# Kernel tuning notes

Hardware: AMD Instinct MI355X
Metric: run time of the kernel (lower is better)

The kernel has to match this reference:

```python
import jax, jax.numpy as jnp
import numpy as np

B, T, C = 4, 2048, 1024
H = 16
D = C // H  # head_dim = 64

def setup_inputs() -> dict:
    key = jax.random.key(0)
    k1, k2, k3 = jax.random.split(key, 3)
    s = 1.0 / np.sqrt(C)
    x = jax.random.normal(k1, (B, T, C), dtype=jnp.float32)
    w_qkv = jax.random.normal(k2, (C, 3 * C), dtype=jnp.float32) * s
    w_proj = jax.random.normal(k3, (C, C), dtype=jnp.float32) * s
    b_proj = jnp.zeros((C,), dtype=jnp.float32)
    return {"x": x, "w_qkv": w_qkv, "w_proj": w_proj, "b_proj": b_proj}

def reference(x, w_qkv, w_proj, b_proj):
    Bc, Tc, Cc = x.shape
    scale = 1.0 / np.sqrt(D)
    qkv = x @ w_qkv                       # [B,T,3C]
    q, k, v = jnp.split(qkv, 3, axis=-1)  # each [B,T,C]
    def heads(t):
        return t.reshape(Bc, Tc, H, D).transpose(0, 2, 1, 3)  # [B,H,T,D]
    q, k, v = heads(q), heads(k), heads(v)
    attn = jnp.einsum('bhqd,bhkd->bhqk', q, k) * scale        # [B,H,T,T]
    causal = jnp.tril(jnp.ones((Tc, Tc), dtype=bool))
    attn = jnp.where(causal, attn, -jnp.inf)
    attn = jax.nn.softmax(attn, axis=-1)
    out = jnp.einsum('bhqk,bhkd->bhqd', attn, v)              # [B,H,T,D]
    out = out.transpose(0, 2, 1, 3).reshape(Bc, Tc, Cc)
    return out @ w_proj + b_proj
```

## Files before the change

kernel.cpp:

```cpp
#include <hip/hip_runtime.h>

typedef unsigned short u16;
typedef unsigned int u32;
typedef __attribute__((ext_vector_type(8))) __bf16 bf16x8;
typedef __attribute__((ext_vector_type(4))) float f32x4;
typedef __attribute__((ext_vector_type(16))) float f32x16;
typedef __attribute__((ext_vector_type(8))) unsigned short ushort8;
typedef __attribute__((ext_vector_type(4))) unsigned short ushort4v;
typedef __attribute__((ext_vector_type(4))) unsigned int u32x4;
typedef __attribute__((ext_vector_type(4))) float float4v;

#define B_ 4
#define T_ 2048
#define C_ 1024
#define H_ 16
#define D_ 64
#define M_ (B_ * T_)

union ABUn { ushort8 u; bf16x8 b; };

__device__ __forceinline__ u16 f2bf(float f) {
  u32 u = __builtin_bit_cast(u32, f);
  u32 r = u + 0x7fffu + ((u >> 16) & 1u);
  return (u16)(r >> 16);
}

__device__ __forceinline__ float fexp2(float x) {
  float r; asm("v_exp_f32 %0, %1" : "=v"(r) : "v"(x)); return r;
}

__device__ __forceinline__ u32 pkbf(float lo, float hi_) {
  u32 r; asm("v_cvt_pk_bf16_f32 %0, %1, %2" : "=v"(r) : "v"(lo), "v"(hi_)); return r;
}

__device__ __forceinline__ void gl16(const u16* g, u16* l) {
  __builtin_amdgcn_global_load_lds((const __attribute__((address_space(1))) void*)g,
                                   (__attribute__((address_space(3))) void*)l, 16, 0, 0);
}

__global__ void cast_kernel(const float* __restrict__ in, u16* __restrict__ out, int n4) {
  int i = blockIdx.x * blockDim.x + threadIdx.x;
  if (i >= n4) return;
  float4v v = ((const float4v*)in)[i];
  ushort4v o;
  o[0] = f2bf(v[0]); o[1] = f2bf(v[1]); o[2] = f2bf(v[2]); o[3] = f2bf(v[3]);
  ((ushort4v*)out)[i] = o;
}

__global__ void transpose_cast_kernel(const float* __restrict__ src, u16* __restrict__ dst,
                                      int Kd, int Nd) {
  __shared__ float tile[32][33];
  int n0 = blockIdx.x * 32, k0 = blockIdx.y * 32;
  int tx = threadIdx.x, ty = threadIdx.y;
#pragma unroll
  for (int i = 0; i < 32; i += 8)
    tile[ty + i][tx] = src[(k0 + ty + i) * Nd + n0 + tx];
  __syncthreads();
#pragma unroll
  for (int i = 0; i < 32; i += 8)
    dst[(n0 + ty + i) * Kd + k0 + tx] = f2bf(tile[tx][ty + i]);
}

template <int EPI>
__global__ __launch_bounds__(256, 2) void gemm_bt(
    const u16* __restrict__ A, const u16* __restrict__ Bt,
    u16* __restrict__ Qb, u16* __restrict__ Kb, u16* __restrict__ Vb,
    float* __restrict__ Out, const float* __restrict__ bias) {
  __shared__ u16 As[128 * 64];
  __shared__ u16 Bs[128 * 64];
  const int tid = threadIdx.x;
  const int lane = tid & 63, wave = tid >> 6;
  const int wm = wave >> 1, wn = wave & 1;
  const int lg = lane >> 4, lr = lane & 15;
  const int m0 = blockIdx.y * 128, n0 = blockIdx.x * 128;

  f32x4 acc[4][4];
  const f32x4 zero = {0.0f, 0.0f, 0.0f, 0.0f};
#pragma unroll
  for (int mi = 0; mi < 4; ++mi)
#pragma unroll
    for (int ni = 0; ni < 4; ++ni) acc[mi][ni] = zero;

  const u16* Abase = A + m0 * 1024;
  const u16* Bbase = Bt + n0 * 1024;
  int aoff[4];
#pragma unroll
  for (int j = 0; j < 4; ++j) {
    int s = wave * 256 + j * 64 + lane;
    int row = s >> 3, sp = s & 7;
    aoff[j] = row * 1024 + (sp ^ (row & 7)) * 8;
  }
  char* AsB = (char*)As;
  char* BsB = (char*)Bs;

  for (int k0 = 0; k0 < 1024; k0 += 64) {
#pragma unroll
    for (int j = 0; j < 4; ++j) {
      u16* ldst_a = &As[(wave * 256 + j * 64) * 8];
      u16* ldst_b = &Bs[(wave * 256 + j * 64) * 8];
      gl16(Abase + aoff[j] + k0, ldst_a);
      gl16(Bbase + aoff[j] + k0, ldst_b);
    }
    __syncthreads();
#pragma unroll
    for (int kk = 0; kk < 2; ++kk) {
      bf16x8 am[4], bn[4];
#pragma unroll
      for (int mi = 0; mi < 4; ++mi) {
        int row = wm * 64 + mi * 16 + lr;
        ABUn u;
        u.u = *(const ushort8*)(AsB + ((u32)(row * 128 + ((kk * 64 + lg * 16) ^ ((row & 7) << 4)))));
        am[mi] = u.b;
      }
#pragma unroll
      for (int ni = 0; ni < 4; ++ni) {
        int row = wn * 64 + ni * 16 + lr;
        ABUn u;
        u.u = *(const ushort8*)(BsB + ((u32)(row * 128 + ((kk * 64 + lg * 16) ^ ((row & 7) << 4)))));
        bn[ni] = u.b;
      }
#pragma unroll
      for (int mi = 0; mi < 4; ++mi)
#pragma unroll
        for (int ni = 0; ni < 4; ++ni)
          acc[mi][ni] = __builtin_amdgcn_mfma_f32_16x16x32_bf16(am[mi], bn[ni], acc[mi][ni], 0, 0, 0);
    }
    __syncthreads();
  }

#pragma unroll
  for (int mi = 0; mi < 4; ++mi)
#pragma unroll
    for (int ni = 0; ni < 4; ++ni) {
      int m = m0 + wm * 64 + mi * 16 + lg * 4;
      int n = n0 + wn * 64 + ni * 16 + lr;
      if (EPI == 0) {
        int part = n >> 10, c = n & 1023;
        int h = c >> 6, d = c & 63;
        int b = m >> 11, t = m & 2047;
        if (part == 2) {
          ushort4v pv;
#pragma unroll
          for (int r = 0; r < 4; ++r) pv[r] = f2bf(acc[mi][ni][r]);
          *(ushort4v*)&Vb[((b * H_ + h) * D_ + d) * T_ + t] = pv;
        } else {
#pragma unroll
          for (int r = 0; r < 4; ++r) {
            float v = acc[mi][ni][r];
            if (part == 0)
              Qb[((b * H_ + h) * T_ + t + r) * D_ + d] = f2bf(v * 0.18033688f);
            else
              Kb[((b * H_ + h) * T_ + t + r) * D_ + d] = f2bf(v);
          }
        }
      } else {
#pragma unroll
        for (int r = 0; r < 4; ++r)
          Out[(m + r) * 1024 + n] = acc[mi][ni][r] + bias[n];
      }
    }
}

__global__ __launch_bounds__(256, 4) void attn_kernel(
    const u16* __restrict__ Qb, const u16* __restrict__ Kb,
    const u16* __restrict__ Vt, u16* __restrict__ Ob) {
  __shared__ u16 smem[4][4096];
  const int bh = blockIdx.y;
  const int tid = threadIdx.x;
  const int lane = tid & 63, wave = tid >> 6;
  const int hi = lane >> 5, ln = lane & 31;
  const int hh = bh & (H_ - 1), bb = bh >> 4;

  const u16* Qh = Qb + bh * (T_ * D_);
  const u16* Kh = Kb + bh * (T_ * D_);
  const u16* Vh = Vt + bh * (T_ * D_);
  const int slot0 = wave * 128;

  int srow[2], scol[2];
#pragma unroll
  for (int j = 0; j < 2; ++j) {
    int slot = slot0 + j * 64 + lane;
    srow[j] = slot >> 3;
    scol[j] = (slot & 7) ^ (srow[j] & 7);
  }

#pragma unroll
  for (int pass = 0; pass < 2; ++pass) {
    const int q0 = pass ? (1920 - (int)blockIdx.x * 128) : ((int)blockIdx.x * 128);
    const int qw0 = q0 + wave * 32;

    bf16x8 qf[4];
    {
      const u16* qr = Qh + (qw0 + ln) * 64 + hi * 8;
#pragma unroll
      for (int ks = 0; ks < 4; ++ks)
        qf[ks] = __builtin_bit_cast(bf16x8, *(const ushort8*)(qr + ks * 16));
    }

    f32x16 o[2];
#pragma unroll
    for (int dt = 0; dt < 2; ++dt)
#pragma unroll
      for (int i = 0; i < 16; ++i) o[dt][i] = 0.0f;
    float m = -1e30f, l = 0.0f;

    const int nchunk = q0 / 64 + 2;

    __syncthreads();
#pragma unroll
    for (int j = 0; j < 2; ++j) {
      gl16(Kh + srow[j] * 64 + scol[j] * 8, &smem[0][(slot0 + j * 64) * 8]);
      gl16(Vh + srow[j] * 2048 + scol[j] * 8, &smem[2][(slot0 + j * 64) * 8]);
    }
    __syncthreads();

    for (int ch = 0; ch < nchunk; ++ch) {
      const int kv0 = ch * 64;
      const int cur = ch & 1;
      if (ch + 1 < nchunk) {
        const int kn = kv0 + 64;
#pragma unroll
        for (int j = 0; j < 2; ++j) {
          gl16(Kh + (kn + srow[j]) * 64 + scol[j] * 8, &smem[cur ^ 1][(slot0 + j * 64) * 8]);
          gl16(Vh + srow[j] * 2048 + kn + scol[j] * 8, &smem[2 + (cur ^ 1)][(slot0 + j * 64) * 8]);
        }
      }
      if (kv0 <= qw0 + 31) {
        const char* Kc = (const char*)smem[cur];
        const char* Vc = (const char*)smem[2 + cur];
        f32x16 s0, s1;
#pragma unroll
        for (int i = 0; i < 16; ++i) { s0[i] = 0.0f; s1[i] = 0.0f; }
        __builtin_amdgcn_s_setprio(1);
#pragma unroll
        for (int ks = 0; ks < 4; ++ks) {
          int r0 = ln, r1 = 32 + ln;
          bf16x8 kf0 = __builtin_bit_cast(bf16x8,
              *(const ushort8*)(Kc + r0 * 128 + (u32)((ks * 32 + hi * 16) ^ ((r0 & 7) << 4))));
          bf16x8 kf1 = __builtin_bit_cast(bf16x8,
              *(const ushort8*)(Kc + r1 * 128 + (u32)((ks * 32 + hi * 16) ^ ((r1 & 7) << 4))));
          s0 = __builtin_amdgcn_mfma_f32_32x32x16_bf16(kf0, qf[ks], s0, 0, 0, 0);
          s1 = __builtin_amdgcn_mfma_f32_32x32x16_bf16(kf1, qf[ks], s1, 0, 0, 0);
        }
        __builtin_amdgcn_s_setprio(0);

        const int qg = qw0 + ln;
        if ((kv0 + 63) > qw0) {
#pragma unroll
          for (int r = 0; r < 16; ++r) {
            int R = (r & 3) + 8 * (r >> 2) + 4 * hi;
            s0[r] = (kv0 + R > qg) ? -1e30f : s0[r];
            s1[r] = (kv0 + 32 + R > qg) ? -1e30f : s1[r];
          }
        }
        float mx[8];
#pragma unroll
        for (int i = 0; i < 8; ++i)
          mx[i] = fmaxf(fmaxf(s0[i], s0[i + 8]), fmaxf(s1[i], s1[i + 8]));
#pragma unroll
        for (int i = 0; i < 4; ++i) mx[i] = fmaxf(mx[i], mx[i + 4]);
        float cm = fmaxf(fmaxf(mx[0], mx[1]), fmaxf(mx[2], mx[3]));
        cm = fmaxf(cm, __shfl_xor(cm, 32));
        float mn = fmaxf(m, cm);
        float fsc = fexp2(m - mn);
        m = mn;
#pragma unroll
        for (int r = 0; r < 16; ++r) {
          s0[r] = fexp2(s0[r] - mn);
          s1[r] = fexp2(s1[r] - mn);
        }
        float sm[8];
#pragma unroll
        for (int i = 0; i < 8; ++i) sm[i] = (s0[i] + s0[i + 8]) + (s1[i] + s1[i + 8]);
#pragma unroll
        for (int i = 0; i < 4; ++i) sm[i] += sm[i + 4];
        float ssum = (sm[0] + sm[1]) + (sm[2] + sm[3]);
        ssum += __shfl_xor(ssum, 32);
        l = l * fsc + ssum;
#pragma unroll
        for (int dt = 0; dt < 2; ++dt)
#pragma unroll
          for (int i = 0; i < 16; ++i) o[dt][i] *= fsc;

        bf16x8 pb[4];
#pragma unroll
        for (int sub = 0; sub < 2; ++sub) {
          u32 a0, a1, a2, a3, a4, a5, a6, a7;
          if (sub == 0) {
            a0 = pkbf(s0[0], s0[1]);  a1 = pkbf(s0[2], s0[3]);
            a2 = pkbf(s0[4], s0[5]);  a3 = pkbf(s0[6], s0[7]);
            a4 = pkbf(s0[8], s0[9]);  a5 = pkbf(s0[10], s0[11]);
            a6 = pkbf(s0[12], s0[13]); a7 = pkbf(s0[14], s0[15]);
          } else {
            a0 = pkbf(s1[0], s1[1]);  a1 = pkbf(s1[2], s1[3]);
            a2 = pkbf(s1[4], s1[5]);  a3 = pkbf(s1[6], s1[7]);
            a4 = pkbf(s1[8], s1[9]);  a5 = pkbf(s1[10], s1[11]);
            a6 = pkbf(s1[12], s1[13]); a7 = pkbf(s1[14], s1[15]);
          }
          asm volatile("v_permlane32_swap_b32 %0, %1" : "+v"(a0), "+v"(a2));
          asm volatile("v_permlane32_swap_b32 %0, %1" : "+v"(a1), "+v"(a3));
          asm volatile("v_permlane32_swap_b32 %0, %1" : "+v"(a4), "+v"(a6));
          asm volatile("v_permlane32_swap_b32 %0, %1" : "+v"(a5), "+v"(a7));
          u32x4 w0, w1;
          w0[0] = a0; w0[1] = a1; w0[2] = a2; w0[3] = a3;
          w1[0] = a4; w1[1] = a5; w1[2] = a6; w1[3] = a7;
          pb[sub * 2 + 0] = __builtin_bit_cast(bf16x8, w0);
          pb[sub * 2 + 1] = __builtin_bit_cast(bf16x8, w1);
        }
        __builtin_amdgcn_s_setprio(1);
#pragma unroll
        for (int dt = 0; dt < 2; ++dt) {
          int r = dt * 32 + ln;
          u32 rs = (u32)((r & 7) << 4);
#pragma unroll
          for (int ks = 0; ks < 4; ++ks) {
            bf16x8 vfk = __builtin_bit_cast(bf16x8,
                *(const ushort8*)(Vc + r * 128 + (u32)((ks * 32 + hi * 16) ^ rs)));
            o[dt] = __builtin_amdgcn_mfma_f32_32x32x16_bf16(vfk, pb[ks], o[dt], 0, 0, 0);
          }
        }
        __builtin_amdgcn_s_setprio(0);
      }
      __syncthreads();
    }

    __syncthreads();
    char* Wb = (char*)smem[wave];
    {
      float inv = 1.0f / l;
      int q = ln;
      u32 rs = (u32)((q & 7) << 4);
#pragma unroll
      for (int dt = 0; dt < 2; ++dt)
#pragma unroll
        for (int p = 0; p < 8; ++p) {
          u32 w = pkbf(o[dt][2 * p] * inv, o[dt][2 * p + 1] * inv);
          int d = dt * 32 + ((2 * p) & 3) + 8 * (p >> 1) + 4 * hi;
          *(u32*)(Wb + ((u32)(q * 128 + d * 2) ^ rs)) = w;
        }
    }
    asm volatile("s_waitcnt lgkmcnt(0)" ::: "memory");
#pragma unroll
    for (int j = 0; j < 4; ++j) {
      int idx = j * 64 + lane;
      int row = idx >> 3, sp = idx & 7;
      ushort8 v = *(const ushort8*)(Wb + row * 128 + (u32)((sp * 16) ^ ((row & 7) << 4)));
      *(ushort8*)(Ob + (bb * T_ + qw0 + row) * C_ + hh * 64 + sp * 8) = v;
    }
  }
}

extern "C" void kernel_launch(void* const* d_in, const int* in_sizes, int n_in,
                              void* d_out, int out_size, void* d_ws, size_t ws_size,
                              hipStream_t stream) {
  const float* x = (const float*)d_in[0];
  const float* w_qkv = (const float*)d_in[1];
  const float* w_proj = (const float*)d_in[2];
  const float* b_proj = (const float*)d_in[3];
  float* out = (float*)d_out;

  char* ws = (char*)d_ws;
  u16* xb = (u16*)(ws);
  u16* wqT = (u16*)(ws + 16777216);
  u16* wpT = (u16*)(ws + 16777216 + 6291456);
  u16* Qb = (u16*)(ws + 25165824);
  u16* Kb = (u16*)(ws + 25165824 + 16777216);
  u16* Vt = (u16*)(ws + 25165824 + 2 * 16777216);
  u16* Ob = xb;

  cast_kernel<<<(M_ * C_ / 4 + 255) / 256, 256, 0, stream>>>(x, xb, M_ * C_ / 4);
  dim3 tb(32, 8);
  transpose_cast_kernel<<<dim3(3 * C_ / 32, C_ / 32), tb, 0, stream>>>(w_qkv, wqT, C_, 3 * C_);
  transpose_cast_kernel<<<dim3(C_ / 32, C_ / 32), tb, 0, stream>>>(w_proj, wpT, C_, C_);

  gemm_bt<0><<<dim3(3 * C_ / 128, M_ / 128), 256, 0, stream>>>(
      xb, wqT, Qb, Kb, Vt, nullptr, nullptr);

  attn_kernel<<<dim3(T_ / 256, B_ * H_), 256, 0, stream>>>(Qb, Kb, Vt, Ob);

  gemm_bt<1><<<dim3(C_ / 128, M_ / 128), 256, 0, stream>>>(
      Ob, wpT, nullptr, nullptr, nullptr, out, b_proj);
}
```

Before: 250.0 us.

## Double attention block to 8 waves and add lazy softmax rescaling

Each attention workgroup now runs 512 threads (8 waves) covering 256 query rows per pass, so each K/V chunk staged into shared memory is shared by twice as many waves, with one load per thread per chunk instead of two. The online softmax skips the max update and the rescale of the output accumulators and row sum unless some lane's chunk max exceeds the running max by more than 8 (in log2 units), which cuts exp and multiply work. The trade-offs are fewer workgroups and more idle waves from causal imbalance inside larger blocks. The lazy rescale also lets unnormalised values grow by up to 2^8 before correction, which is safe in fp32 but changes the numerics slightly.

```diff
diff --git a/kernel.cpp b/kernel.cpp
--- a/kernel.cpp
+++ b/kernel.cpp
@@ -161,7 +161,7 @@
     }
 }
 
-__global__ __launch_bounds__(256, 4) void attn_kernel(
+__global__ __launch_bounds__(512, 4) void attn_kernel(
     const u16* __restrict__ Qb, const u16* __restrict__ Kb,
     const u16* __restrict__ Vt, u16* __restrict__ Ob) {
   __shared__ u16 smem[4][4096];
@@ -174,19 +174,14 @@
   const u16* Qh = Qb + bh * (T_ * D_);
   const u16* Kh = Kb + bh * (T_ * D_);
   const u16* Vh = Vt + bh * (T_ * D_);
-  const int slot0 = wave * 128;
-
-  int srow[2], scol[2];
-#pragma unroll
-  for (int j = 0; j < 2; ++j) {
-    int slot = slot0 + j * 64 + lane;
-    srow[j] = slot >> 3;
-    scol[j] = (slot & 7) ^ (srow[j] & 7);
-  }
+
+  const int srow = tid >> 3;
+  const int scol = (tid & 7) ^ (srow & 7);
+  u16* kdst = &smem[0][(wave * 64) * 8];
 
 #pragma unroll
   for (int pass = 0; pass < 2; ++pass) {
-    const int q0 = pass ? (1920 - (int)blockIdx.x * 128) : ((int)blockIdx.x * 128);
+    const int q0 = pass ? (1792 - (int)blockIdx.x * 256) : ((int)blockIdx.x * 256);
     const int qw0 = q0 + wave * 32;
 
     bf16x8 qf[4];
@@ -204,14 +199,11 @@
       for (int i = 0; i < 16; ++i) o[dt][i] = 0.0f;
     float m = -1e30f, l = 0.0f;
 
-    const int nchunk = q0 / 64 + 2;
-
-    __syncthreads();
-#pragma unroll
-    for (int j = 0; j < 2; ++j) {
-      gl16(Kh + srow[j] * 64 + scol[j] * 8, &smem[0][(slot0 + j * 64) * 8]);
-      gl16(Vh + srow[j] * 2048 + scol[j] * 8, &smem[2][(slot0 + j * 64) * 8]);
-    }
+    const int nchunk = q0 / 64 + 4;
+
+    __syncthreads();
+    gl16(Kh + srow * 64 + scol * 8, kdst);
+    gl16(Vh + srow * 2048 + scol * 8, kdst + 2 * 4096);
     __syncthreads();
 
     for (int ch = 0; ch < nchunk; ++ch) {
@@ -219,11 +211,8 @@
       const int cur = ch & 1;
       if (ch + 1 < nchunk) {
         const int kn = kv0 + 64;
-#pragma unroll
-        for (int j = 0; j < 2; ++j) {
-          gl16(Kh + (kn + srow[j]) * 64 + scol[j] * 8, &smem[cur ^ 1][(slot0 + j * 64) * 8]);
-          gl16(Vh + srow[j] * 2048 + kn + scol[j] * 8, &smem[2 + (cur ^ 1)][(slot0 + j * 64) * 8]);
-        }
+        gl16(Kh + (kn + srow) * 64 + scol * 8, kdst + (cur ^ 1) * 4096);
+        gl16(Vh + srow * 2048 + kn + scol * 8, kdst + (2 + (cur ^ 1)) * 4096);
       }
       if (kv0 <= qw0 + 31) {
         const char* Kc = (const char*)smem[cur];
@@ -261,13 +250,20 @@
         for (int i = 0; i < 4; ++i) mx[i] = fmaxf(mx[i], mx[i + 4]);
         float cm = fmaxf(fmaxf(mx[0], mx[1]), fmaxf(mx[2], mx[3]));
         cm = fmaxf(cm, __shfl_xor(cm, 32));
-        float mn = fmaxf(m, cm);
-        float fsc = fexp2(m - mn);
-        m = mn;
+        if (!__all(cm <= m + 8.0f)) {
+          float mn = fmaxf(m, cm);
+          float fsc = fexp2(m - mn);
+          m = mn;
+          l *= fsc;
+#pragma unroll
+          for (int dt = 0; dt < 2; ++dt)
+#pragma unroll
+            for (int i = 0; i < 16; ++i) o[dt][i] *= fsc;
+        }
 #pragma unroll
         for (int r = 0; r < 16; ++r) {
-          s0[r] = fexp2(s0[r] - mn);
-          s1[r] = fexp2(s1[r] - mn);
+          s0[r] = fexp2(s0[r] - m);
+          s1[r] = fexp2(s1[r] - m);
         }
         float sm[8];
 #pragma unroll
@@ -276,11 +272,7 @@
         for (int i = 0; i < 4; ++i) sm[i] += sm[i + 4];
         float ssum = (sm[0] + sm[1]) + (sm[2] + sm[3]);
         ssum += __shfl_xor(ssum, 32);
-        l = l * fsc + ssum;
-#pragma unroll
-        for (int dt = 0; dt < 2; ++dt)
-#pragma unroll
-          for (int i = 0; i < 16; ++i) o[dt][i] *= fsc;
+        l += ssum;
 
         bf16x8 pb[4];
 #pragma unroll
@@ -325,7 +317,7 @@
     }
 
     __syncthreads();
-    char* Wb = (char*)smem[wave];
+    char* Wb = ((char*)smem) + wave * 4096;
     {
       float inv = 1.0f / l;
       int q = ln;
@@ -376,7 +368,7 @@
   gemm_bt<0><<<dim3(3 * C_ / 128, M_ / 128), 256, 0, stream>>>(
       xb, wqT, Qb, Kb, Vt, nullptr, nullptr);
 
-  attn_kernel<<<dim3(T_ / 256, B_ * H_), 256, 0, stream>>>(Qb, Kb, Vt, Ob);
+  attn_kernel<<<dim3(T_ / 512, B_ * H_), 512, 0, stream>>>(Qb, Kb, Vt, Ob);
 
   gemm_bt<1><<<dim3(C_ / 128, M_ / 128), 256, 0, stream>>>(
       Ob, wpT, nullptr, nullptr, nullptr, out, b_proj);
```

After: 234.1 us. 1.07x faster.
